# Kernel tuning notes

Measured on AMD Instinct MI355X. Metric: run time of the kernel, lower is better.

Reference implementation:

```python
import jax, jax.numpy as jnp
import numpy as np

H_RES, W_RES = 256, 256
HIDDEN = 128


def setup_inputs() -> dict:
    key = jax.random.key(0)
    ks = jax.random.split(key, 10)

    def xavier(k, fan_out, fan_in):
        lim = np.sqrt(6.0 / (fan_in + fan_out)).astype(np.float32)
        return jax.random.uniform(k, (fan_out, fan_in), jnp.float32, -lim, lim)

    B, C, P = 16, 16, 8
    return {
        "bezier_points": jax.random.uniform(ks[0], (B, C, P, 2), jnp.float32),
        "W1": xavier(ks[1], 64, 2),   "b1": jnp.zeros((64,), jnp.float32),
        "W2": xavier(ks[2], HIDDEN, 64), "b2": jnp.zeros((HIDDEN,), jnp.float32),
        "W3": xavier(ks[3], HIDDEN, HIDDEN), "b3": jnp.zeros((HIDDEN,), jnp.float32),
        "Wf": xavier(ks[4], 2, HIDDEN), "bf": jnp.zeros((2,), jnp.float32),
        "kde_bandwidth": jnp.float32(0.1),
        "density_threshold": jnp.float32(0.5),
    }


def reference(bezier_points, W1, b1, W2, b2, W3, b3, Wf, bf,
              kde_bandwidth, density_threshold):
    B = bezier_points.shape[0]
    pts = bezier_points.reshape(B, -1, 2)          # [B, N, 2]
    N = pts.shape[1]

    # point encoder MLP (Linear-ReLU-Linear-ReLU-Linear)
    h = jax.nn.relu(pts @ W1.T + b1)
    h = jax.nn.relu(h @ W2.T + b2)
    enc = h @ W3.T + b3                            # [B, N, HIDDEN]
    vecs = enc @ Wf.T + bf                         # [B, N, 2] field vectors

    # dense [-1,1]^2 grid, points stored as (x, y)
    y = jnp.linspace(-1.0, 1.0, H_RES)
    x = jnp.linspace(-1.0, 1.0, W_RES)
    gy, gx = jnp.meshgrid(y, x, indexing="ij")
    grid = jnp.stack([gx, gy], axis=-1).reshape(-1, 2)   # [HW, 2]

    # squared distances grid<->points via ||g||^2 + ||p||^2 - 2 g.p  -> [B, HW, N]
    gn = jnp.sum(grid * grid, axis=-1)             # [HW]
    pn = jnp.sum(pts * pts, axis=-1)               # [B, N]
    d2 = jnp.maximum(gn[None, :, None] + pn[:, None, :]
                     - 2.0 * jnp.einsum("gd,bnd->bgn", grid, pts), 0.0)

    bw = jnp.maximum(kde_bandwidth, 1e-5)

    # KDE density: sum of gaussians, normalized, sigmoid-thresholded
    dens = jnp.exp(-0.5 * d2 / (bw * bw)).sum(-1) / (N * bw * jnp.sqrt(2.0 * jnp.pi))
    density_map = jax.nn.sigmoid(dens - density_threshold).reshape(B, 1, H_RES, W_RES)

    # control field: zero-points are skipped (torch.allclose(point, 0), atol=1e-8)
    valid = jnp.any(jnp.abs(pts) > 1e-8, axis=-1).astype(d2.dtype)   # [B, N]
    wf = jnp.exp(-(d2 + 1e-8) / (2.0 * bw * bw)) * valid[:, None, :]  # [B, HW, N]
    field = jnp.tanh(jnp.einsum("bgn,bnc->bgc", wf, vecs))            # [B, HW, 2]
    field_map = field.reshape(B, H_RES, W_RES, 2).transpose(0, 3, 1, 2)  # [B,2,H,W]

    return density_map, field_map
```

## Files before the change

### kernel.cpp

```cpp
#include <hip/hip_runtime.h>
#include <math.h>

#define LOG2E   1.4426950408889634f
#define SQRT2PI 2.5066282746310002f

typedef _Float16 half8 __attribute__((ext_vector_type(8)));
typedef float    f32x4 __attribute__((ext_vector_type(4)));

__device__ __forceinline__ float tanh_fast(float z) {
  float az = fabsf(z);
  float u  = exp2f(-2.0f * LOG2E * az);
  float r  = (1.0f - u) / (1.0f + u);
  return copysignf(r, z);
}

#define DOT4(acc, a, h)                                      \
  acc = fmaf((a).x, (h).x, acc); acc = fmaf((a).y, (h).y, acc); \
  acc = fmaf((a).z, (h).z, acc); acc = fmaf((a).w, (h).w, acc);

__global__ __launch_bounds__(256) void mlp_kernel(
    const float* __restrict__ pts,
    const float* __restrict__ W1, const float* __restrict__ b1,
    const float* __restrict__ W2, const float* __restrict__ b2,
    const float* __restrict__ W3, const float* __restrict__ b3,
    const float* __restrict__ Wf, const float* __restrict__ bf,
    const float* __restrict__ bw_p,
    float* __restrict__ wpx, float* __restrict__ wpy,
    float* __restrict__ wvx, float* __restrict__ wvy)
{
  __shared__ float sp[8][2];
  __shared__ float sh1[8][64];
  __shared__ float sh2[8][128];
  __shared__ float sh3[8][128];
  const int tid = threadIdx.x;
  const int p0  = blockIdx.x * 8;

  if (tid < 16) sp[tid >> 1][tid & 1] = pts[(p0 + (tid >> 1)) * 2 + (tid & 1)];
  __syncthreads();

  for (int t = tid; t < 8 * 64; t += 256) {
    int pt = t >> 6, o = t & 63;
    float h = fmaf(W1[o * 2 + 1], sp[pt][1], fmaf(W1[o * 2], sp[pt][0], b1[o]));
    sh1[pt][o] = fmaxf(h, 0.0f);
  }
  __syncthreads();

  {
    const int o = tid & 127, g = tid >> 7;
    float4 w[16];
    const float4* wrow = (const float4*)(W2 + o * 64);
#pragma unroll
    for (int i = 0; i < 16; ++i) w[i] = wrow[i];
    const float bb = b2[o];
#pragma unroll
    for (int k = 0; k < 4; ++k) {
      const int pt = g * 4 + k;
      const float4* h4 = (const float4*)(&sh1[pt][0]);
      float acc = bb;
#pragma unroll
      for (int i = 0; i < 16; ++i) { float4 hh = h4[i]; DOT4(acc, w[i], hh); }
      sh2[pt][o] = fmaxf(acc, 0.0f);
    }
  }
  __syncthreads();

  {
    const int o = tid & 127, g = tid >> 7;
    float4 w[32];
    const float4* wrow = (const float4*)(W3 + o * 128);
#pragma unroll
    for (int i = 0; i < 32; ++i) w[i] = wrow[i];
    const float bb = b3[o];
#pragma unroll
    for (int k = 0; k < 4; ++k) {
      const int pt = g * 4 + k;
      const float4* h4 = (const float4*)(&sh2[pt][0]);
      float acc = bb;
#pragma unroll
      for (int i = 0; i < 32; ++i) { float4 hh = h4[i]; DOT4(acc, w[i], hh); }
      sh3[pt][o] = acc;
    }
  }
  __syncthreads();

  if (tid < 16) {
    const int pt = tid >> 1, c = tid & 1;
    float acc = bf[c];
    const float4* wv = (const float4*)(Wf + c * 128);
    const float4* h4 = (const float4*)(&sh3[pt][0]);
#pragma unroll
    for (int i = 0; i < 32; ++i) { float4 a = wv[i]; float4 hh = h4[i]; DOT4(acc, a, hh); }
    const float px = sp[pt][0], py = sp[pt][1];
    const bool valid = (fabsf(px) > 1e-8f) || (fabsf(py) > 1e-8f);
    const float bw = fmaxf(bw_p[0], 1e-5f);
    const float K  = expf(-1e-8f / (2.0f * bw * bw));
    const float v  = valid ? acc * K : 0.0f;
    const int gp = p0 + pt;
    if (c == 0) { wvx[gp] = v; wpx[gp] = px; wpy[gp] = py; }
    else        { wvy[gp] = v; }
  }
}

__global__ __launch_bounds__(256) void tablegen_kernel(
    const float* __restrict__ wpx, const float* __restrict__ wpy,
    const float* __restrict__ wvx, const float* __restrict__ wvy,
    const float* __restrict__ bw_p,
    _Float16* __restrict__ Eyt, _Float16* __restrict__ Vxt,
    _Float16* __restrict__ Vyt, _Float16* __restrict__ Ext)
{
  const int b   = blockIdx.x >> 4;
  const int seg = blockIdx.x & 15;
  const int pr  = threadIdx.x >> 4;
  const int ng  = threadIdx.x & 15;
  const int pix = seg * 16 + pr;
  const float bw = fmaxf(bw_p[0], 1e-5f);
  const float c2 = -0.5f / (bw * bw) * LOG2E;
  const float STEP = 2.0f / 255.0f;
  const float g = fmaf((float)pix, STEP, -1.0f);
  const int nb = b * 128 + ng * 8;

  float px8[8], py8[8], vx8[8], vy8[8];
  *(float4*)&px8[0] = *(const float4*)&wpx[nb];
  *(float4*)&px8[4] = *(const float4*)&wpx[nb + 4];
  *(float4*)&py8[0] = *(const float4*)&wpy[nb];
  *(float4*)&py8[4] = *(const float4*)&wpy[nb + 4];
  *(float4*)&vx8[0] = *(const float4*)&wvx[nb];
  *(float4*)&vx8[4] = *(const float4*)&wvx[nb + 4];
  *(float4*)&vy8[0] = *(const float4*)&wvy[nb];
  *(float4*)&vy8[4] = *(const float4*)&wvy[nb + 4];

  half8 ey, vxe, vye, ex;
#pragma unroll
  for (int i = 0; i < 8; ++i) {
    const float dy = g - py8[i];
    const float e  = exp2f(c2 * dy * dy);
    ey[i]  = (_Float16)e;
    vxe[i] = (_Float16)(e * vx8[i]);
    vye[i] = (_Float16)(e * vy8[i]);
    const float dx = g - px8[i];
    ex[i]  = (_Float16)exp2f(c2 * dx * dx);
  }
  const size_t base = ((size_t)b * 256 + pix) * 128 + ng * 8;
  *(half8*)&Eyt[base] = ey;
  *(half8*)&Vxt[base] = vxe;
  *(half8*)&Vyt[base] = vye;
  *(half8*)&Ext[base] = ex;
}

__global__ __launch_bounds__(256) void field_mfma_kernel(
    const _Float16* __restrict__ Eyt, const _Float16* __restrict__ Vxt,
    const _Float16* __restrict__ Vyt, const _Float16* __restrict__ Ext,
    const float* __restrict__ bw_p, const float* __restrict__ thr_p,
    float* __restrict__ out)
{
  const int bid = blockIdx.x;
  const int b   = bid >> 5;
  const int yt  = (bid >> 1) & 15;
  const int xt  = bid & 1;
  const int wv   = threadIdx.x >> 6;
  const int lane = threadIdx.x & 63;
  const int lr = lane & 15, lg = lane >> 4;
  const int y0 = yt * 16;
  const int x0 = xt * 128 + wv * 32;

  const size_t tb   = (size_t)b * 256 * 128;
  const size_t arow = tb + (size_t)(y0 + lr) * 128 + lg * 8;
  const _Float16* pEy = Eyt + arow;
  const _Float16* pVx = Vxt + arow;
  const _Float16* pVy = Vyt + arow;
  const size_t brow0 = tb + (size_t)(x0 + lr) * 128 + lg * 8;
  const size_t brow1 = brow0 + 16 * 128;

  f32x4 acc[3][2];
#pragma unroll
  for (int c = 0; c < 3; ++c)
#pragma unroll
    for (int n = 0; n < 2; ++n) acc[c][n] = (f32x4){0.f, 0.f, 0.f, 0.f};

#pragma unroll
  for (int kk = 0; kk < 4; ++kk) {
    const int ko = kk * 32;
    const half8 aE = *(const half8*)(pEy + ko);
    const half8 aX = *(const half8*)(pVx + ko);
    const half8 aY = *(const half8*)(pVy + ko);
    const half8 b0 = *(const half8*)(Ext + brow0 + ko);
    const half8 b1 = *(const half8*)(Ext + brow1 + ko);
    acc[0][0] = __builtin_amdgcn_mfma_f32_16x16x32_f16(aE, b0, acc[0][0], 0, 0, 0);
    acc[1][0] = __builtin_amdgcn_mfma_f32_16x16x32_f16(aX, b0, acc[1][0], 0, 0, 0);
    acc[2][0] = __builtin_amdgcn_mfma_f32_16x16x32_f16(aY, b0, acc[2][0], 0, 0, 0);
    acc[0][1] = __builtin_amdgcn_mfma_f32_16x16x32_f16(aE, b1, acc[0][1], 0, 0, 0);
    acc[1][1] = __builtin_amdgcn_mfma_f32_16x16x32_f16(aX, b1, acc[1][1], 0, 0, 0);
    acc[2][1] = __builtin_amdgcn_mfma_f32_16x16x32_f16(aY, b1, acc[2][1], 0, 0, 0);
  }

  const float bw  = fmaxf(bw_p[0], 1e-5f);
  const float thr = thr_p[0];
  const float inv_norm = 1.0f / (128.0f * bw * SQRT2PI);
  float* outD = out;
  float* outF = out + (size_t)16 * 65536;

#pragma unroll
  for (int nt = 0; nt < 2; ++nt) {
    const int x = x0 + nt * 16 + lr;
#pragma unroll
    for (int r = 0; r < 4; ++r) {
      const int y = y0 + lg * 4 + r;
      const size_t pidx = (size_t)y * 256 + x;
      const float dn = acc[0][nt][r] * inv_norm;
      outD[(size_t)b * 65536 + pidx] = 1.0f / (1.0f + exp2f((thr - dn) * LOG2E));
      outF[(size_t)b * 131072 + pidx]         = tanh_fast(acc[1][nt][r]);
      outF[(size_t)b * 131072 + 65536 + pidx] = tanh_fast(acc[2][nt][r]);
    }
  }
}

extern "C" void kernel_launch(void* const* d_in, const int* in_sizes, int n_in,
                              void* d_out, int out_size, void* d_ws, size_t ws_size,
                              hipStream_t stream) {
  const float* pts = (const float*)d_in[0];
  const float* W1  = (const float*)d_in[1];
  const float* b1  = (const float*)d_in[2];
  const float* W2  = (const float*)d_in[3];
  const float* b2  = (const float*)d_in[4];
  const float* W3  = (const float*)d_in[5];
  const float* b3  = (const float*)d_in[6];
  const float* Wf  = (const float*)d_in[7];
  const float* bf  = (const float*)d_in[8];
  const float* bw  = (const float*)d_in[9];
  const float* thr = (const float*)d_in[10];

  float* ws  = (float*)d_ws;
  float* wpx = ws;
  float* wpy = ws + 2048;
  float* wvx = ws + 4096;
  float* wvy = ws + 6144;
  _Float16* Eyt = (_Float16*)(ws + 8192);
  _Float16* Vxt = Eyt + 524288;
  _Float16* Vyt = Vxt + 524288;
  _Float16* Ext = Vyt + 524288;

  hipLaunchKernelGGL(mlp_kernel, dim3(256), dim3(256), 0, stream,
                     pts, W1, b1, W2, b2, W3, b3, Wf, bf, bw,
                     wpx, wpy, wvx, wvy);

  hipLaunchKernelGGL(tablegen_kernel, dim3(256), dim3(256), 0, stream,
                     wpx, wpy, wvx, wvy, bw, Eyt, Vxt, Vyt, Ext);

  hipLaunchKernelGGL(field_mfma_kernel, dim3(512), dim3(256), 0, stream,
                     Eyt, Vxt, Vyt, Ext, bw, thr, (float*)d_out);
}
```

Measured before the change: 29.38 us.

## Fuse table generation into MLP kernel and use fast reciprocals

The separate tablegen kernel is folded into the MLP kernel. Each block now owns 8 points of one batch and writes that slice of the per-row Gaussian/value tables for all 256 grid coordinates, which removes one kernel launch and the workspace round trip for the point and vector arrays. The layer 2 and 3 loops are reordered so each weight float4 is reused across the 4 points. Divisions in tanh and sigmoid are replaced with hardware approximate reciprocals, which can cost a little precision.

```diff
diff --git a/kernel.cpp b/kernel.cpp
--- a/kernel.cpp
+++ b/kernel.cpp
@@ -6,34 +6,39 @@
 
 typedef _Float16 half8 __attribute__((ext_vector_type(8)));
 typedef float    f32x4 __attribute__((ext_vector_type(4)));
+
+__device__ __forceinline__ float rcp_fast(float x) { return __builtin_amdgcn_rcpf(x); }
 
 __device__ __forceinline__ float tanh_fast(float z) {
   float az = fabsf(z);
   float u  = exp2f(-2.0f * LOG2E * az);
-  float r  = (1.0f - u) / (1.0f + u);
+  float r  = (1.0f - u) * rcp_fast(1.0f + u);
   return copysignf(r, z);
 }
 
-#define DOT4(acc, a, h)                                      \
+#define DOT4(acc, a, h)                                        \
   acc = fmaf((a).x, (h).x, acc); acc = fmaf((a).y, (h).y, acc); \
   acc = fmaf((a).z, (h).z, acc); acc = fmaf((a).w, (h).w, acc);
 
-__global__ __launch_bounds__(256) void mlp_kernel(
+__global__ __launch_bounds__(256) void mlp_table_kernel(
     const float* __restrict__ pts,
     const float* __restrict__ W1, const float* __restrict__ b1,
     const float* __restrict__ W2, const float* __restrict__ b2,
     const float* __restrict__ W3, const float* __restrict__ b3,
     const float* __restrict__ Wf, const float* __restrict__ bf,
     const float* __restrict__ bw_p,
-    float* __restrict__ wpx, float* __restrict__ wpy,
-    float* __restrict__ wvx, float* __restrict__ wvy)
+    _Float16* __restrict__ Eyt, _Float16* __restrict__ Vxt,
+    _Float16* __restrict__ Vyt, _Float16* __restrict__ Ext)
 {
   __shared__ float sp[8][2];
   __shared__ float sh1[8][64];
   __shared__ float sh2[8][128];
   __shared__ float sh3[8][128];
+  __shared__ float sfin[8][2];
   const int tid = threadIdx.x;
-  const int p0  = blockIdx.x * 8;
+  const int b   = blockIdx.x >> 4;
+  const int q   = blockIdx.x & 15;
+  const int p0  = b * 128 + q * 8;
 
   if (tid < 16) sp[tid >> 1][tid & 1] = pts[(p0 + (tid >> 1)) * 2 + (tid & 1)];
   __syncthreads();
@@ -51,16 +56,20 @@
     const float4* wrow = (const float4*)(W2 + o * 64);
 #pragma unroll
     for (int i = 0; i < 16; ++i) w[i] = wrow[i];
-    const float bb = b2[o];
-#pragma unroll
-    for (int k = 0; k < 4; ++k) {
-      const int pt = g * 4 + k;
-      const float4* h4 = (const float4*)(&sh1[pt][0]);
-      float acc = bb;
-#pragma unroll
-      for (int i = 0; i < 16; ++i) { float4 hh = h4[i]; DOT4(acc, w[i], hh); }
-      sh2[pt][o] = fmaxf(acc, 0.0f);
-    }
+    float acc[4];
+#pragma unroll
+    for (int j = 0; j < 4; ++j) acc[j] = b2[o];
+#pragma unroll
+    for (int i = 0; i < 16; ++i) {
+      const float4 ww = w[i];
+#pragma unroll
+      for (int j = 0; j < 4; ++j) {
+        const float4 hh = *(const float4*)&sh1[g * 4 + j][i * 4];
+        DOT4(acc[j], ww, hh);
+      }
+    }
+#pragma unroll
+    for (int j = 0; j < 4; ++j) sh2[g * 4 + j][o] = fmaxf(acc[j], 0.0f);
   }
   __syncthreads();
 
@@ -70,16 +79,20 @@
     const float4* wrow = (const float4*)(W3 + o * 128);
 #pragma unroll
     for (int i = 0; i < 32; ++i) w[i] = wrow[i];
-    const float bb = b3[o];
-#pragma unroll
-    for (int k = 0; k < 4; ++k) {
-      const int pt = g * 4 + k;
-      const float4* h4 = (const float4*)(&sh2[pt][0]);
-      float acc = bb;
-#pragma unroll
-      for (int i = 0; i < 32; ++i) { float4 hh = h4[i]; DOT4(acc, w[i], hh); }
-      sh3[pt][o] = acc;
-    }
+    float acc[4];
+#pragma unroll
+    for (int j = 0; j < 4; ++j) acc[j] = b3[o];
+#pragma unroll
+    for (int i = 0; i < 32; ++i) {
+      const float4 ww = w[i];
+#pragma unroll
+      for (int j = 0; j < 4; ++j) {
+        const float4 hh = *(const float4*)&sh2[g * 4 + j][i * 4];
+        DOT4(acc[j], ww, hh);
+      }
+    }
+#pragma unroll
+    for (int j = 0; j < 4; ++j) sh3[g * 4 + j][o] = acc[j];
   }
   __syncthreads();
 
@@ -87,64 +100,39 @@
     const int pt = tid >> 1, c = tid & 1;
     float acc = bf[c];
     const float4* wv = (const float4*)(Wf + c * 128);
-    const float4* h4 = (const float4*)(&sh3[pt][0]);
+    const float4* h4 = (const float4*)&sh3[pt][0];
 #pragma unroll
     for (int i = 0; i < 32; ++i) { float4 a = wv[i]; float4 hh = h4[i]; DOT4(acc, a, hh); }
     const float px = sp[pt][0], py = sp[pt][1];
     const bool valid = (fabsf(px) > 1e-8f) || (fabsf(py) > 1e-8f);
     const float bw = fmaxf(bw_p[0], 1e-5f);
     const float K  = expf(-1e-8f / (2.0f * bw * bw));
-    const float v  = valid ? acc * K : 0.0f;
-    const int gp = p0 + pt;
-    if (c == 0) { wvx[gp] = v; wpx[gp] = px; wpy[gp] = py; }
-    else        { wvy[gp] = v; }
-  }
-}
-
-__global__ __launch_bounds__(256) void tablegen_kernel(
-    const float* __restrict__ wpx, const float* __restrict__ wpy,
-    const float* __restrict__ wvx, const float* __restrict__ wvy,
-    const float* __restrict__ bw_p,
-    _Float16* __restrict__ Eyt, _Float16* __restrict__ Vxt,
-    _Float16* __restrict__ Vyt, _Float16* __restrict__ Ext)
-{
-  const int b   = blockIdx.x >> 4;
-  const int seg = blockIdx.x & 15;
-  const int pr  = threadIdx.x >> 4;
-  const int ng  = threadIdx.x & 15;
-  const int pix = seg * 16 + pr;
-  const float bw = fmaxf(bw_p[0], 1e-5f);
-  const float c2 = -0.5f / (bw * bw) * LOG2E;
-  const float STEP = 2.0f / 255.0f;
-  const float g = fmaf((float)pix, STEP, -1.0f);
-  const int nb = b * 128 + ng * 8;
-
-  float px8[8], py8[8], vx8[8], vy8[8];
-  *(float4*)&px8[0] = *(const float4*)&wpx[nb];
-  *(float4*)&px8[4] = *(const float4*)&wpx[nb + 4];
-  *(float4*)&py8[0] = *(const float4*)&wpy[nb];
-  *(float4*)&py8[4] = *(const float4*)&wpy[nb + 4];
-  *(float4*)&vx8[0] = *(const float4*)&wvx[nb];
-  *(float4*)&vx8[4] = *(const float4*)&wvx[nb + 4];
-  *(float4*)&vy8[0] = *(const float4*)&wvy[nb];
-  *(float4*)&vy8[4] = *(const float4*)&wvy[nb + 4];
-
-  half8 ey, vxe, vye, ex;
-#pragma unroll
-  for (int i = 0; i < 8; ++i) {
-    const float dy = g - py8[i];
-    const float e  = exp2f(c2 * dy * dy);
-    ey[i]  = (_Float16)e;
-    vxe[i] = (_Float16)(e * vx8[i]);
-    vye[i] = (_Float16)(e * vy8[i]);
-    const float dx = g - px8[i];
-    ex[i]  = (_Float16)exp2f(c2 * dx * dx);
-  }
-  const size_t base = ((size_t)b * 256 + pix) * 128 + ng * 8;
-  *(half8*)&Eyt[base] = ey;
-  *(half8*)&Vxt[base] = vxe;
-  *(half8*)&Vyt[base] = vye;
-  *(half8*)&Ext[base] = ex;
+    sfin[pt][c] = valid ? acc * K : 0.0f;
+  }
+  __syncthreads();
+
+  {
+    const float bw = fmaxf(bw_p[0], 1e-5f);
+    const float c2 = -0.5f / (bw * bw) * LOG2E;
+    const float STEP = 2.0f / 255.0f;
+    const float g = fmaf((float)tid, STEP, -1.0f);
+    half8 ey, vxe, vye, ex;
+#pragma unroll
+    for (int j = 0; j < 8; ++j) {
+      const float dy = g - sp[j][1];
+      const float e  = exp2f(c2 * dy * dy);
+      ey[j]  = (_Float16)e;
+      vxe[j] = (_Float16)(e * sfin[j][0]);
+      vye[j] = (_Float16)(e * sfin[j][1]);
+      const float dx = g - sp[j][0];
+      ex[j]  = (_Float16)exp2f(c2 * dx * dx);
+    }
+    const size_t base = ((size_t)b * 256 + tid) * 128 + q * 8;
+    *(half8*)&Eyt[base] = ey;
+    *(half8*)&Vxt[base] = vxe;
+    *(half8*)&Vyt[base] = vye;
+    *(half8*)&Ext[base] = ex;
+  }
 }
 
 __global__ __launch_bounds__(256) void field_mfma_kernel(
@@ -207,7 +195,7 @@
       const int y = y0 + lg * 4 + r;
       const size_t pidx = (size_t)y * 256 + x;
       const float dn = acc[0][nt][r] * inv_norm;
-      outD[(size_t)b * 65536 + pidx] = 1.0f / (1.0f + exp2f((thr - dn) * LOG2E));
+      outD[(size_t)b * 65536 + pidx] = rcp_fast(1.0f + exp2f((thr - dn) * LOG2E));
       outF[(size_t)b * 131072 + pidx]         = tanh_fast(acc[1][nt][r]);
       outF[(size_t)b * 131072 + 65536 + pidx] = tanh_fast(acc[2][nt][r]);
     }
@@ -229,22 +217,14 @@
   const float* bw  = (const float*)d_in[9];
   const float* thr = (const float*)d_in[10];
 
-  float* ws  = (float*)d_ws;
-  float* wpx = ws;
-  float* wpy = ws + 2048;
-  float* wvx = ws + 4096;
-  float* wvy = ws + 6144;
-  _Float16* Eyt = (_Float16*)(ws + 8192);
+  _Float16* Eyt = (_Float16*)d_ws;
   _Float16* Vxt = Eyt + 524288;
   _Float16* Vyt = Vxt + 524288;
   _Float16* Ext = Vyt + 524288;
 
-  hipLaunchKernelGGL(mlp_kernel, dim3(256), dim3(256), 0, stream,
+  hipLaunchKernelGGL(mlp_table_kernel, dim3(256), dim3(256), 0, stream,
                      pts, W1, b1, W2, b2, W3, b3, Wf, bf, bw,
-                     wpx, wpy, wvx, wvy);
-
-  hipLaunchKernelGGL(tablegen_kernel, dim3(256), dim3(256), 0, stream,
-                     wpx, wpy, wvx, wvy, bw, Eyt, Vxt, Vyt, Ext);
+                     Eyt, Vxt, Vyt, Ext);
 
   hipLaunchKernelGGL(field_mfma_kernel, dim3(512), dim3(256), 0, stream,
                      Eyt, Vxt, Vyt, Ext, bw, thr, (float*)d_out);
```

New measurement: 27.66 us. 5.9% less time.
